# Kernel tuning notes

Measured on AMD Instinct MI355X. Metric: run time of the kernel, lower is better.

## Reference

```python
import jax, jax.numpy as jnp
import numpy as np

N = 65536          # number of input vectors
D = 128            # embedding_dim
K = 2048           # num_embeddings (codebook size)
DH = D // 2        # linear_proj output dim


def setup_inputs() -> dict:
    key = jax.random.key(0)
    k1, k2, k3, k4 = jax.random.split(key, 4)
    z = jax.random.normal(k1, (N, D), dtype=jnp.float32)
    # linear_proj params (nn.Linear(D, D//2)): weight [DH, D], bias [DH]
    W = jax.random.normal(k2, (DH, D), dtype=jnp.float32) * (1.0 / np.sqrt(D))
    b = jax.random.normal(k3, (DH,), dtype=jnp.float32) * 0.01
    # codebook buffer, initialized ~ N(0,1) as in the torch module
    embeddings = jax.random.normal(k4, (K, D), dtype=jnp.float32)
    return {"z": z, "W": W, "b": b, "embeddings": embeddings}


def reference(z, W, b, embeddings):
    # project inputs and codebook into half-dim space
    z_ = z @ W.T + b                       # [N, DH]
    emb_ = embeddings @ W.T + b            # [K, DH]
    # squared euclidean distances via ||a||^2 + ||b||^2 - 2 a.b
    distances = ((z_ ** 2).sum(-1, keepdims=True)
                 + (emb_ ** 2).sum(-1)
                 - 2.0 * (z_ @ emb_.T))    # [N, K]
    closest = jnp.argmin(distances, axis=-1)               # [N]
    one_hot_encoding = jax.nn.one_hot(closest, K, dtype=jnp.float32)  # [N, K]
    quantized = one_hot_encoding @ embeddings               # [N, D] (gather)
    return (quantized, one_hot_encoding)
```

## Files before the change

### kernel.cpp

```cpp
#include <hip/hip_runtime.h>
#include <float.h>

#define N_ROWS 65536
#define D_IN   128
#define DH     64
#define K_CB   2048

typedef const __attribute__((address_space(1))) void* gas_p;
typedef __attribute__((address_space(3))) void* las_p;
typedef __bf16 bf16x8 __attribute__((ext_vector_type(8)));
typedef float  f32x4  __attribute__((ext_vector_type(4)));

__global__ __launch_bounds__(256) void k_project(
    const float* __restrict__ Z, const float* __restrict__ emb,
    const float* __restrict__ W, const float* __restrict__ b,
    __bf16* __restrict__ zpl,
    __bf16* __restrict__ epl,
    float* __restrict__ e2) {
  __shared__ __align__(16) float Wl[64 * 140];
  __shared__ __align__(16) float Zl[16 * 128];
  int tid = threadIdx.x;
  const float* src; __bf16* dst; int n0; bool do_e2; size_t plane;
  if ((int)blockIdx.x < 4096) {
    src = Z;   dst = zpl; n0 = blockIdx.x * 16;          do_e2 = false; plane = (size_t)N_ROWS * 64;
  } else {
    src = emb; dst = epl; n0 = (blockIdx.x - 4096) * 16; do_e2 = true;  plane = (size_t)K_CB * 64;
  }

#pragma unroll
  for (int i = 0; i < 8; ++i) {
    int idx4 = tid + 256 * i;
    int j = idx4 >> 5;
    int d4 = (idx4 & 31) * 4;
    *(float4*)&Wl[j * 140 + d4] = *(const float4*)(W + j * 128 + d4);
  }
#pragma unroll
  for (int i = 0; i < 2; ++i) {
    int idx4 = tid + 256 * i;
    int r = idx4 >> 5;
    int d4 = (idx4 & 31) * 4;
    *(float4*)&Zl[r * 128 + d4] = *(const float4*)(src + (size_t)(n0 + r) * 128 + d4);
  }
  int j = tid & 63, g = tid >> 6;
  float bj = b[j];
  __syncthreads();

  float acc[4] = {0.f, 0.f, 0.f, 0.f};
  for (int d4 = 0; d4 < 128; d4 += 4) {
    float4 w4 = *(float4*)&Wl[j * 140 + d4];
#pragma unroll
    for (int i = 0; i < 4; ++i) {
      float4 z4 = *(float4*)&Zl[(g * 4 + i) * 128 + d4];
      acc[i] = fmaf(z4.x, w4.x, fmaf(z4.y, w4.y, fmaf(z4.z, w4.z, fmaf(z4.w, w4.w, acc[i]))));
    }
  }
#pragma unroll
  for (int i = 0; i < 4; ++i) {
    int n = n0 + g * 4 + i;
    float v = acc[i] + bj;
    __bf16 h = (__bf16)v;  float rm = v - (float)h;
    __bf16 m = (__bf16)rm; float rl = rm - (float)m;
    __bf16 l = (__bf16)rl;
    int pos = (((j >> 3) ^ (n & 7)) << 3) | (j & 7);
    size_t base = (size_t)n * 64 + pos;
    dst[base]             = h;
    dst[plane + base]     = m;
    dst[2 * plane + base] = l;
    if (do_e2) {
      float s = v * v;
#pragma unroll
      for (int off = 32; off > 0; off >>= 1) s += __shfl_xor(s, off, 64);
      if (j == 0) e2[n] = s;
    }
  }
}

__global__ __launch_bounds__(256, 2) void k_score(
    const __bf16* __restrict__ zpl,
    const __bf16* __restrict__ epl,
    const float* __restrict__ e2,
    const float* __restrict__ emb,
    float* __restrict__ outQ,
    float* __restrict__ outOH,
    int* __restrict__ cidx_g) {
  __shared__ __align__(16) __bf16 Zs[3 * 64 * 64];
  __shared__ __align__(16) __bf16 Es[3 * 128 * 64];
  __shared__ float e2s[128];

  int tid = threadIdx.x, lane = tid & 63, wid = tid >> 6;
  int quad = lane >> 4, l16 = lane & 15;
  int wcol = wid * 32;
  int row0 = blockIdx.x * 64;

  for (int q = wid; q < 24; q += 4) {
    int p = q >> 3, within = (q & 7) * 1024;
    const char* g = (const char*)zpl + (size_t)p * ((size_t)N_ROWS * 128)
                  + (size_t)row0 * 128 + within + lane * 16;
    __builtin_amdgcn_global_load_lds((gas_p)g, (las_p)((char*)Zs + p * 8192 + within), 16, 0, 0);
  }

  float best[16]; int bidx[16];
#pragma unroll
  for (int s = 0; s < 16; ++s) { best[s] = FLT_MAX; bidx[s] = 0; }

  for (int kt = 0; kt < K_CB; kt += 128) {
    __syncthreads();
    for (int q = wid; q < 48; q += 4) {
      int p = q >> 4, within = (q & 15) * 1024;
      const char* g = (const char*)epl + (size_t)p * (K_CB * 128)
                    + (size_t)kt * 128 + within + lane * 16;
      __builtin_amdgcn_global_load_lds((gas_p)g, (las_p)((char*)Es + p * 16384 + within), 16, 0, 0);
    }
    if (tid < 128) e2s[tid] = e2[kt + tid];
    if (outOH) {
      float4 zz = make_float4(0.f, 0.f, 0.f, 0.f);
#pragma unroll
      for (int i = 0; i < 8; ++i) {
        int idx = tid + 256 * i;
        int r = idx >> 5, c4 = (idx & 31) * 4;
        *(float4*)(outOH + (size_t)(row0 + r) * K_CB + kt + c4) = zz;
      }
    }
    __syncthreads();

    f32x4 accf[4][2];
#pragma unroll
    for (int mt = 0; mt < 4; ++mt)
#pragma unroll
      for (int nt = 0; nt < 2; ++nt) accf[mt][nt] = (f32x4){0.f, 0.f, 0.f, 0.f};

#pragma unroll
    for (int step = 0; step < 2; ++step) {
      bf16x8 A[4][3];
#pragma unroll
      for (int mt = 0; mt < 4; ++mt) {
        int tr = mt * 16 + l16;
        int cph = (step * 4 + quad) ^ (tr & 7);
        const __bf16* pa = Zs + tr * 64 + cph * 8;
        A[mt][0] = *(const bf16x8*)pa;
        A[mt][1] = *(const bf16x8*)(pa + 4096);
        A[mt][2] = *(const bf16x8*)(pa + 8192);
      }
#pragma unroll
      for (int nt = 0; nt < 2; ++nt) {
        int tc = wcol + nt * 16 + l16;
        int cph = (step * 4 + quad) ^ (tc & 7);
        const __bf16* pb = Es + tc * 64 + cph * 8;
        bf16x8 Bh = *(const bf16x8*)pb;
        bf16x8 Bm = *(const bf16x8*)(pb + 8192);
        bf16x8 Bl = *(const bf16x8*)(pb + 16384);
#pragma unroll
        for (int mt = 0; mt < 4; ++mt) {
          f32x4 c = accf[mt][nt];
          c = __builtin_amdgcn_mfma_f32_16x16x32_bf16(A[mt][2], Bh, c, 0, 0, 0);
          c = __builtin_amdgcn_mfma_f32_16x16x32_bf16(A[mt][0], Bl, c, 0, 0, 0);
          c = __builtin_amdgcn_mfma_f32_16x16x32_bf16(A[mt][1], Bm, c, 0, 0, 0);
          c = __builtin_amdgcn_mfma_f32_16x16x32_bf16(A[mt][1], Bh, c, 0, 0, 0);
          c = __builtin_amdgcn_mfma_f32_16x16x32_bf16(A[mt][0], Bm, c, 0, 0, 0);
          c = __builtin_amdgcn_mfma_f32_16x16x32_bf16(A[mt][0], Bh, c, 0, 0, 0);
          accf[mt][nt] = c;
        }
      }
    }

#pragma unroll
    for (int nt = 0; nt < 2; ++nt) {
      float ev = e2s[wcol + nt * 16 + l16];
      int col = kt + wcol + nt * 16 + l16;
#pragma unroll
      for (int mt = 0; mt < 4; ++mt)
#pragma unroll
        for (int r = 0; r < 4; ++r) {
          float s = fmaf(-2.0f, accf[mt][nt][r], ev);
          int slot = mt * 4 + r;
          if (s < best[slot]) { best[slot] = s; bidx[slot] = col; }
        }
    }
  }

  __syncthreads();
  float* redm = (float*)Es;
  int*   redi = (int*)((char*)Es + 16384);
#pragma unroll
  for (int mt = 0; mt < 4; ++mt)
#pragma unroll
    for (int r = 0; r < 4; ++r) {
      int row = mt * 16 + quad * 4 + r;
      redm[row * 64 + wid * 16 + l16] = best[mt * 4 + r];
      redi[row * 64 + wid * 16 + l16] = bidx[mt * 4 + r];
    }
  __syncthreads();
  int* cidx = (int*)Zs;
  if (tid < 64) {
    float m = redm[tid * 64]; int mi = redi[tid * 64];
    for (int s = 1; s < 64; ++s) {
      float v = redm[tid * 64 + s]; int vi = redi[tid * 64 + s];
      if (v < m || (v == m && vi < mi)) { m = v; mi = vi; }
    }
    cidx[tid] = mi;
  }
  __syncthreads();

  if (outOH) {
    if (tid < 64) outOH[(size_t)(row0 + tid) * K_CB + cidx[tid]] = 1.0f;
  } else {
    if (tid < 64) cidx_g[row0 + tid] = cidx[tid];
  }

#pragma unroll
  for (int i = 0; i < 8; ++i) {
    int idx = tid + 256 * i;
    int r = idx >> 5, c = (idx & 31) * 4;
    *(float4*)(outQ + (size_t)(row0 + r) * D_IN + c) =
        *(const float4*)(emb + (size_t)cidx[r] * D_IN + c);
  }
}

__global__ void k_epilogue(const int* __restrict__ cidx_g, float* __restrict__ outOH) {
  int tid  = threadIdx.x;
  int row0 = blockIdx.x * 64;
  float4 zz4 = make_float4(0.f, 0.f, 0.f, 0.f);
  for (int r = 0; r < 64; ++r) {
    float4* dst = (float4*)(outOH + (size_t)(row0 + r) * K_CB);
    dst[tid]       = zz4;
    dst[tid + 256] = zz4;
  }
  __syncthreads();
  if (tid < 64) {
    int r = row0 + tid;
    outOH[(size_t)r * K_CB + cidx_g[r]] = 1.0f;
  }
}

extern "C" void kernel_launch(void* const* d_in, const int* in_sizes, int n_in,
                              void* d_out, int out_size, void* d_ws, size_t ws_size,
                              hipStream_t stream) {
  (void)in_sizes; (void)n_in; (void)out_size;
  const float* Z   = (const float*)d_in[0];
  const float* W   = (const float*)d_in[1];
  const float* b   = (const float*)d_in[2];
  const float* emb = (const float*)d_in[3];
  float* outQ  = (float*)d_out;
  float* outOH = (float*)d_out + (size_t)N_ROWS * D_IN;

  char* wsb = (char*)d_ws;
  __bf16* epl = (__bf16*)wsb;
  float*  e2  = (float*)(wsb + 786432);
  const size_t need_primary = 786432 + 8192 + (size_t)3 * N_ROWS * 64 * 2;

  if (ws_size >= need_primary) {
    __bf16* zpl = (__bf16*)(wsb + 794624);
    k_project<<<4224, 256, 0, stream>>>(Z, emb, W, b, zpl, epl, e2);
    k_score<<<1024, 256, 0, stream>>>(zpl, epl, e2, emb, outQ, outOH, nullptr);
  } else {
    int*    cidx_g = (int*)(wsb + 794624);
    __bf16* zpl    = (__bf16*)outOH;
    k_project<<<4224, 256, 0, stream>>>(Z, emb, W, b, zpl, epl, e2);
    k_score<<<1024, 256, 0, stream>>>(zpl, epl, e2, emb, outQ, nullptr, cidx_g);
    k_epilogue<<<1024, 256, 0, stream>>>(cidx_g, outOH);
  }
}
```

Measured before the change: 702.3 us.

## Switch split-precision distance GEMM from 3-plane bf16 to 2-plane fp16

Replaces the three-term bf16 split of projected vectors with a two-term fp16 split, cutting the cross-product MFMAs per tile from six to four and shrinking the plane storage and LDS tiles by a third. The smaller LDS footprint allows raising launch bounds to three blocks per CU. The one-hot zeroing stores now sit after the load barrier instead of overlapping the codebook fetch. The fp16 hi+lo split has less dynamic range and lower total precision than three bf16 terms, so near-tie argmin choices may differ.

```diff
diff --git a/kernel.cpp b/kernel.cpp
--- a/kernel.cpp
+++ b/kernel.cpp
@@ -8,19 +8,19 @@
 
 typedef const __attribute__((address_space(1))) void* gas_p;
 typedef __attribute__((address_space(3))) void* las_p;
-typedef __bf16 bf16x8 __attribute__((ext_vector_type(8)));
-typedef float  f32x4  __attribute__((ext_vector_type(4)));
+typedef _Float16 f16x8 __attribute__((ext_vector_type(8)));
+typedef float    f32x4 __attribute__((ext_vector_type(4)));
 
 __global__ __launch_bounds__(256) void k_project(
     const float* __restrict__ Z, const float* __restrict__ emb,
     const float* __restrict__ W, const float* __restrict__ b,
-    __bf16* __restrict__ zpl,
-    __bf16* __restrict__ epl,
+    _Float16* __restrict__ zpl,
+    _Float16* __restrict__ epl,
     float* __restrict__ e2) {
   __shared__ __align__(16) float Wl[64 * 140];
   __shared__ __align__(16) float Zl[16 * 128];
   int tid = threadIdx.x;
-  const float* src; __bf16* dst; int n0; bool do_e2; size_t plane;
+  const float* src; _Float16* dst; int n0; bool do_e2; size_t plane;
   if ((int)blockIdx.x < 4096) {
     src = Z;   dst = zpl; n0 = blockIdx.x * 16;          do_e2 = false; plane = (size_t)N_ROWS * 64;
   } else {
@@ -58,14 +58,12 @@
   for (int i = 0; i < 4; ++i) {
     int n = n0 + g * 4 + i;
     float v = acc[i] + bj;
-    __bf16 h = (__bf16)v;  float rm = v - (float)h;
-    __bf16 m = (__bf16)rm; float rl = rm - (float)m;
-    __bf16 l = (__bf16)rl;
+    _Float16 h = (_Float16)v;  float rm = v - (float)h;
+    _Float16 m = (_Float16)rm;
     int pos = (((j >> 3) ^ (n & 7)) << 3) | (j & 7);
     size_t base = (size_t)n * 64 + pos;
-    dst[base]             = h;
-    dst[plane + base]     = m;
-    dst[2 * plane + base] = l;
+    dst[base]         = h;
+    dst[plane + base] = m;
     if (do_e2) {
       float s = v * v;
 #pragma unroll
@@ -75,16 +73,16 @@
   }
 }
 
-__global__ __launch_bounds__(256, 2) void k_score(
-    const __bf16* __restrict__ zpl,
-    const __bf16* __restrict__ epl,
+__global__ __launch_bounds__(256, 3) void k_score(
+    const _Float16* __restrict__ zpl,
+    const _Float16* __restrict__ epl,
     const float* __restrict__ e2,
     const float* __restrict__ emb,
     float* __restrict__ outQ,
     float* __restrict__ outOH,
     int* __restrict__ cidx_g) {
-  __shared__ __align__(16) __bf16 Zs[3 * 64 * 64];
-  __shared__ __align__(16) __bf16 Es[3 * 128 * 64];
+  __shared__ __align__(16) _Float16 Zs[2 * 64 * 64];
+  __shared__ __align__(16) _Float16 Es[2 * 128 * 64];
   __shared__ float e2s[128];
 
   int tid = threadIdx.x, lane = tid & 63, wid = tid >> 6;
@@ -92,7 +90,7 @@
   int wcol = wid * 32;
   int row0 = blockIdx.x * 64;
 
-  for (int q = wid; q < 24; q += 4) {
+  for (int q = wid; q < 16; q += 4) {
     int p = q >> 3, within = (q & 7) * 1024;
     const char* g = (const char*)zpl + (size_t)p * ((size_t)N_ROWS * 128)
                   + (size_t)row0 * 128 + within + lane * 16;
@@ -105,13 +103,15 @@
 
   for (int kt = 0; kt < K_CB; kt += 128) {
     __syncthreads();
-    for (int q = wid; q < 48; q += 4) {
+    for (int q = wid; q < 32; q += 4) {
       int p = q >> 4, within = (q & 15) * 1024;
       const char* g = (const char*)epl + (size_t)p * (K_CB * 128)
                     + (size_t)kt * 128 + within + lane * 16;
       __builtin_amdgcn_global_load_lds((gas_p)g, (las_p)((char*)Es + p * 16384 + within), 16, 0, 0);
     }
     if (tid < 128) e2s[tid] = e2[kt + tid];
+    __syncthreads();
+
     if (outOH) {
       float4 zz = make_float4(0.f, 0.f, 0.f, 0.f);
 #pragma unroll
@@ -121,7 +121,6 @@
         *(float4*)(outOH + (size_t)(row0 + r) * K_CB + kt + c4) = zz;
       }
     }
-    __syncthreads();
 
     f32x4 accf[4][2];
 #pragma unroll
@@ -131,33 +130,29 @@
 
 #pragma unroll
     for (int step = 0; step < 2; ++step) {
-      bf16x8 A[4][3];
+      f16x8 A[4][2];
 #pragma unroll
       for (int mt = 0; mt < 4; ++mt) {
         int tr = mt * 16 + l16;
         int cph = (step * 4 + quad) ^ (tr & 7);
-        const __bf16* pa = Zs + tr * 64 + cph * 8;
-        A[mt][0] = *(const bf16x8*)pa;
-        A[mt][1] = *(const bf16x8*)(pa + 4096);
-        A[mt][2] = *(const bf16x8*)(pa + 8192);
+        const _Float16* pa = Zs + tr * 64 + cph * 8;
+        A[mt][0] = *(const f16x8*)pa;
+        A[mt][1] = *(const f16x8*)(pa + 4096);
       }
 #pragma unroll
       for (int nt = 0; nt < 2; ++nt) {
         int tc = wcol + nt * 16 + l16;
         int cph = (step * 4 + quad) ^ (tc & 7);
-        const __bf16* pb = Es + tc * 64 + cph * 8;
-        bf16x8 Bh = *(const bf16x8*)pb;
-        bf16x8 Bm = *(const bf16x8*)(pb + 8192);
-        bf16x8 Bl = *(const bf16x8*)(pb + 16384);
+        const _Float16* pb = Es + tc * 64 + cph * 8;
+        f16x8 Bh = *(const f16x8*)pb;
+        f16x8 Bm = *(const f16x8*)(pb + 8192);
 #pragma unroll
         for (int mt = 0; mt < 4; ++mt) {
           f32x4 c = accf[mt][nt];
-          c = __builtin_amdgcn_mfma_f32_16x16x32_bf16(A[mt][2], Bh, c, 0, 0, 0);
-          c = __builtin_amdgcn_mfma_f32_16x16x32_bf16(A[mt][0], Bl, c, 0, 0, 0);
-          c = __builtin_amdgcn_mfma_f32_16x16x32_bf16(A[mt][1], Bm, c, 0, 0, 0);
-          c = __builtin_amdgcn_mfma_f32_16x16x32_bf16(A[mt][1], Bh, c, 0, 0, 0);
-          c = __builtin_amdgcn_mfma_f32_16x16x32_bf16(A[mt][0], Bm, c, 0, 0, 0);
-          c = __builtin_amdgcn_mfma_f32_16x16x32_bf16(A[mt][0], Bh, c, 0, 0, 0);
+          c = __builtin_amdgcn_mfma_f32_16x16x32_f16(A[mt][1], Bm, c, 0, 0, 0);
+          c = __builtin_amdgcn_mfma_f32_16x16x32_f16(A[mt][1], Bh, c, 0, 0, 0);
+          c = __builtin_amdgcn_mfma_f32_16x16x32_f16(A[mt][0], Bm, c, 0, 0, 0);
+          c = __builtin_amdgcn_mfma_f32_16x16x32_f16(A[mt][0], Bh, c, 0, 0, 0);
           accf[mt][nt] = c;
         }
       }
@@ -244,17 +239,17 @@
   float* outOH = (float*)d_out + (size_t)N_ROWS * D_IN;
 
   char* wsb = (char*)d_ws;
-  __bf16* epl = (__bf16*)wsb;
-  float*  e2  = (float*)(wsb + 786432);
-  const size_t need_primary = 786432 + 8192 + (size_t)3 * N_ROWS * 64 * 2;
+  _Float16* epl = (_Float16*)wsb;
+  float*    e2  = (float*)(wsb + 524288);
+  const size_t need_primary = 524288 + 8192 + (size_t)2 * N_ROWS * 64 * 2;
 
   if (ws_size >= need_primary) {
-    __bf16* zpl = (__bf16*)(wsb + 794624);
+    _Float16* zpl = (_Float16*)(wsb + 532480);
     k_project<<<4224, 256, 0, stream>>>(Z, emb, W, b, zpl, epl, e2);
     k_score<<<1024, 256, 0, stream>>>(zpl, epl, e2, emb, outQ, outOH, nullptr);
   } else {
-    int*    cidx_g = (int*)(wsb + 794624);
-    __bf16* zpl    = (__bf16*)outOH;
+    int*      cidx_g = (int*)(wsb + 532480);
+    _Float16* zpl    = (_Float16*)outOH;
     k_project<<<4224, 256, 0, stream>>>(Z, emb, W, b, zpl, epl, e2);
     k_score<<<1024, 256, 0, stream>>>(zpl, epl, e2, emb, outQ, nullptr, cidx_g);
     k_epilogue<<<1024, 256, 0, stream>>>(cidx_g, outOH);
```

After: 689.6 us. Within noise of the previous version (-1.8%).
